# Optimization experiments

Measured on AMD Instinct MI355X. Metric: run time of the kernel, lower is better.

Reference implementation:

```python
import jax, jax.numpy as jnp
import numpy as np

B = 524288
IN_DIM = 16
OUT_DIM = 32  # hidden_dim3
N_CHUNKS = 4
CHUNK = 4


def ste_round(x):
    # straight-through round (grad passes unchanged, like Round.apply)
    return x + jax.lax.stop_gradient(jnp.round(x) - x)


def ste_sign(x):
    # straight-through sign (grad passes unchanged, like Sign.apply)
    return x + jax.lax.stop_gradient(jnp.sign(x) - x)


def setup_inputs() -> dict:
    key = jax.random.key(0)
    k1, k2 = jax.random.split(key)
    Input = jax.random.uniform(k1, (B, IN_DIM), dtype=jnp.float32)
    weight = jax.random.normal(k2, (OUT_DIM, IN_DIM), dtype=jnp.float32)
    InMin = jnp.float32(0.0)
    InMax = jnp.float32(1.0)
    return {"Input": Input, "weight": weight, "InMin": InMin, "InMax": InMax}


def reference(Input, weight, InMin, InMax):
    # eval-mode forward of QuantLinear
    scale = InMax - InMin
    w = ste_sign(weight)                       # [O, I] in {-1, 0, 1}
    wP = jax.nn.relu(w)                        # positive mask
    wM = jax.nn.relu(-w)                       # negative mask

    # 4-bit input quantization (eval path): clip(round((x-min)/(max-min)*15), 0, 15)
    q = jnp.clip(ste_round((Input - InMin) / scale * 15.0), 0.0, 15.0)  # [B, I]

    # bias = linear(InMin * ones, w): each row = InMin * sum_j w[o, j]
    bias = InMin * jnp.sum(w, axis=1)          # [O], broadcasts over batch

    # chunked 4-wide linears, vectorized over the 4 chunks
    qc = q.reshape(B, N_CHUNKS, CHUNK)         # [B, C, 4]
    wPc = wP.reshape(OUT_DIM, N_CHUNKS, CHUNK)  # [O, C, 4]
    wMc = wM.reshape(OUT_DIM, N_CHUNKS, CHUNK)
    yP = jnp.einsum('bcf,ocf->cbo', qc, wPc)   # [C, B, O]
    yM = jnp.einsum('bcf,ocf->cbo', qc, wMc)   # [C, B, O]

    # accumulate clip(round(y/15), -4, 4) * (InMax - InMin) over all 8 terms
    terms = jnp.clip(ste_round(yP / 15.0), -4.0, 4.0) \
          + jnp.clip(ste_round(-yM / 15.0), -4.0, 4.0)  # [C, B, O]
    x = jnp.sum(terms, axis=0) * scale + bias  # [B, O]
    return x
```

## Files before the change

### kernel.cpp

```cpp
#include <hip/hip_runtime.h>
#include <stdint.h>


#if __has_builtin(__builtin_amdgcn_udot4)
#define HAVE_UDOT4 1
#else
#define HAVE_UDOT4 0
#endif

typedef float f32x4 __attribute__((ext_vector_type(4)));

__device__ __forceinline__ int rnd15(int x) {
    return (int)(__umul24((unsigned)x, 274u) >> 12);
}

#if HAVE_UDOT4
#define TERM(q, mp, mm)                                                     \
    (rnd15((int)__builtin_amdgcn_udot4((q), (mp), 7u, false)) -             \
     rnd15((int)__builtin_amdgcn_udot4((q), (mm), 7u, false)))
#else
#define BSUM(x) ((int)((uint32_t)((x) * 0x01010101u) >> 24))
#define TERM(q, mp, mm)                                                     \
    (rnd15(BSUM((q) & (mp)) + 7) - rnd15(BSUM((q) & (mm)) + 7))
#endif

__global__ __launch_bounds__(256) void qlin_main(
    const float* __restrict__ in, const float* __restrict__ wgt,
    const float* __restrict__ pmin, const float* __restrict__ pmax,
    float* __restrict__ out, int nrows)
{
    __shared__ __align__(16) uint32_t cmP[128];
    __shared__ __align__(16) uint32_t cmM[128];
    __shared__ __align__(16) float sbias[32];
    __shared__ __align__(16) uint32_t xpose[256];

    const int t = threadIdx.x;
    const int lane = t & 63;
    const int wv = t >> 6;
    const size_t R0 = ((size_t)blockIdx.x * 4 + wv) * 64;
    (void)nrows;

    const float4* inp = (const float4*)in + R0 * 4 + lane;
    float4 f0 = inp[0], f1 = inp[64], f2 = inp[128], f3 = inp[192];

    const uint32_t MB = HAVE_UDOT4 ? 1u : 0xFFu;

    if (t < 128) {
        const int o = t >> 2, c = t & 3;
        const float* wrow = wgt + o * 16 + c * 4;
        uint32_t mp = 0, mm = 0;
#pragma unroll
        for (int j = 0; j < 4; ++j) {
            float v = wrow[j];
            if (v > 0.0f) mp |= MB << (8 * j);
            if (v < 0.0f) mm |= MB << (8 * j);
        }
        cmP[t] = mp;
        cmM[t] = mm;
    }
    if (t < 32) {
        const float* wrow = wgt + t * 16;
        int s = 0;
#pragma unroll
        for (int j = 0; j < 16; ++j) {
            float v = wrow[j];
            s += (v > 0.0f) ? 1 : 0;
            s -= (v < 0.0f) ? 1 : 0;
        }
        sbias[t] = __fmul_rn(pmin[0], (float)s);
    }
    __syncthreads();

    const int ogrp = lane & 7;
    const int rsel = lane >> 3;
    uint32_t* xp = xpose + (wv << 6);

    const uint4 P0 = *(const uint4*)&cmP[(ogrp * 4 + 0) * 4];
    const uint4 P1 = *(const uint4*)&cmP[(ogrp * 4 + 1) * 4];
    const uint4 P2 = *(const uint4*)&cmP[(ogrp * 4 + 2) * 4];
    const uint4 P3 = *(const uint4*)&cmP[(ogrp * 4 + 3) * 4];
    const uint4 M0 = *(const uint4*)&cmM[(ogrp * 4 + 0) * 4];
    const uint4 M1 = *(const uint4*)&cmM[(ogrp * 4 + 1) * 4];
    const uint4 M2 = *(const uint4*)&cmM[(ogrp * 4 + 2) * 4];
    const uint4 M3 = *(const uint4*)&cmM[(ogrp * 4 + 3) * 4];
    const float4 bias = *(const float4*)(sbias + ogrp * 4);

    const float InMin = pmin[0];
    const float scale = __fsub_rn(pmax[0], InMin);
    const bool unit =
        (__builtin_amdgcn_readfirstlane(__float_as_uint(scale)) == 0x3f800000u);

#define QUANT1(EJ, PK, J)                                                   \
        {                                                                   \
            float v  = __fmul_rn(EJ, 15.0f);                                \
            float rr = rintf(v);                                            \
            rr = fminf(fmaxf(rr, 0.0f), 15.0f);                             \
            PK |= ((uint32_t)(int)rr) << (8 * (J));                         \
        }

#define QUANT(F, QW)                                                        \
    {                                                                       \
        uint32_t pk = 0;                                                    \
        if (unit) {                                                         \
            QUANT1(__fsub_rn(F.x, InMin), pk, 0)                            \
            QUANT1(__fsub_rn(F.y, InMin), pk, 1)                            \
            QUANT1(__fsub_rn(F.z, InMin), pk, 2)                            \
            QUANT1(__fsub_rn(F.w, InMin), pk, 3)                            \
        } else {                                                            \
            QUANT1(__fdiv_rn(__fsub_rn(F.x, InMin), scale), pk, 0)          \
            QUANT1(__fdiv_rn(__fsub_rn(F.y, InMin), scale), pk, 1)          \
            QUANT1(__fdiv_rn(__fsub_rn(F.z, InMin), scale), pk, 2)          \
            QUANT1(__fdiv_rn(__fsub_rn(F.w, InMin), scale), pk, 3)          \
        }                                                                   \
        QW = pk;                                                            \
    }

#define ROWCOMP(q0, q1, q2, q3, dst)                                        \
        {                                                                   \
            int a0 = TERM(q0, P0.x, M0.x) + TERM(q1, P0.y, M0.y)            \
                   + TERM(q2, P0.z, M0.z) + TERM(q3, P0.w, M0.w);           \
            int a1 = TERM(q0, P1.x, M1.x) + TERM(q1, P1.y, M1.y)            \
                   + TERM(q2, P1.z, M1.z) + TERM(q3, P1.w, M1.w);           \
            int a2 = TERM(q0, P2.x, M2.x) + TERM(q1, P2.y, M2.y)            \
                   + TERM(q2, P2.z, M2.z) + TERM(q3, P2.w, M2.w);           \
            int a3 = TERM(q0, P3.x, M3.x) + TERM(q1, P3.y, M3.y)            \
                   + TERM(q2, P3.z, M3.z) + TERM(q3, P3.w, M3.w);           \
            f32x4 res;                                                      \
            res.x = __fadd_rn(__fmul_rn((float)a0, scale), bias.x);         \
            res.y = __fadd_rn(__fmul_rn((float)a1, scale), bias.y);         \
            res.z = __fadd_rn(__fmul_rn((float)a2, scale), bias.z);         \
            res.w = __fadd_rn(__fmul_rn((float)a3, scale), bias.w);         \
            __builtin_nontemporal_store(res, (f32x4*)(dst));                \
        }

#define SLAB(F, K)                                                          \
    {                                                                       \
        uint32_t qw;                                                        \
        QUANT(F, qw);                                                       \
        xp[lane] = qw;                                                      \
        const uint4 qA = *(const uint4*)(xp + (rsel << 2));                 \
        const uint4 qB = *(const uint4*)(xp + 32 + (rsel << 2));            \
        float* p0 = out + (R0 + (size_t)(K) * 16 + rsel) * 32 + (ogrp << 2);\
        ROWCOMP(qA.x, qA.y, qA.z, qA.w, p0);                                \
        ROWCOMP(qB.x, qB.y, qB.z, qB.w, p0 + 256);                          \
    }

    SLAB(f0, 0)
    SLAB(f1, 1)
    SLAB(f2, 2)
    SLAB(f3, 3)

#undef SLAB
#undef ROWCOMP
#undef QUANT
#undef QUANT1
}

extern "C" void kernel_launch(void* const* d_in, const int* in_sizes, int n_in,
                              void* d_out, int out_size, void* d_ws, size_t ws_size,
                              hipStream_t stream) {
    (void)n_in; (void)d_ws; (void)ws_size; (void)out_size;
    const float* in  = (const float*)d_in[0];
    const float* wgt = (const float*)d_in[1];
    const float* mn  = (const float*)d_in[2];
    const float* mx  = (const float*)d_in[3];
    float* out = (float*)d_out;
    const int nrows = in_sizes[0] / 16;
    const int blocks = nrows / 256;
    qlin_main<<<blocks, 256, 0, stream>>>(in, wgt, mn, mx, out, nrows);
}
```

Before: 100.5 us.

## Fold round-by-15 into udot4 weights and build per-wave masks without block barrier

Pre-scales the quantized inputs by 2 and uses 137 as each mask byte, so one udot4 with a folded bias constant plus a shift replaces the separate multiply-shift rounding step. Each wavefront now builds its own copy of the weight masks and the bias (computed with popcount) in shared memory, which removes the block-wide __syncthreads at the cost of redundant setup work and more LDS. Output stores also change from nontemporal to plain stores. The new exact-division trick relies on the udot4 sums staying small enough to avoid overflow and on the rounding identity holding across the full 0..60 range.

Result: no change. 98.63 us, median of 2 (-1.9%).

```diff
diff --git a/kernel.cpp b/kernel.cpp
--- a/kernel.cpp
+++ b/kernel.cpp
@@ -10,18 +10,23 @@
 
 typedef float f32x4 __attribute__((ext_vector_type(4)));
 
-__device__ __forceinline__ int rnd15(int x) {
+#if HAVE_UDOT4
+#define TERM(q2, mp, mm)                                                    \
+    ((int)(__builtin_amdgcn_udot4((q2), (mp), 1918u, false) >> 12) -        \
+     (int)(__builtin_amdgcn_udot4((q2), (mm), 1918u, false) >> 12))
+#define MBYTE 137u
+#define QSH 1
+#define BPB 3
+#else
+#define BSUM(x) ((int)((uint32_t)((x) * 0x01010101u) >> 24))
+__device__ __forceinline__ int rnd15f(int x) {
     return (int)(__umul24((unsigned)x, 274u) >> 12);
 }
-
-#if HAVE_UDOT4
 #define TERM(q, mp, mm)                                                     \
-    (rnd15((int)__builtin_amdgcn_udot4((q), (mp), 7u, false)) -             \
-     rnd15((int)__builtin_amdgcn_udot4((q), (mm), 7u, false)))
-#else
-#define BSUM(x) ((int)((uint32_t)((x) * 0x01010101u) >> 24))
-#define TERM(q, mp, mm)                                                     \
-    (rnd15(BSUM((q) & (mp)) + 7) - rnd15(BSUM((q) & (mm)) + 7))
+    (rnd15f(BSUM((q) & (mp)) + 7) - rnd15f(BSUM((q) & (mm)) + 7))
+#define MBYTE 0xFFu
+#define QSH 0
+#define BPB 8
 #endif
 
 __global__ __launch_bounds__(256) void qlin_main(
@@ -29,10 +34,10 @@
     const float* __restrict__ pmin, const float* __restrict__ pmax,
     float* __restrict__ out, int nrows)
 {
-    __shared__ __align__(16) uint32_t cmP[128];
-    __shared__ __align__(16) uint32_t cmM[128];
-    __shared__ __align__(16) float sbias[32];
-    __shared__ __align__(16) uint32_t xpose[256];
+    __shared__ __align__(16) uint32_t sP[4][128];
+    __shared__ __align__(16) uint32_t sM[4][128];
+    __shared__ __align__(16) float    sB[4][32];
+    __shared__ __align__(16) uint32_t sX[4][64];
 
     const int t = threadIdx.x;
     const int lane = t & 63;
@@ -43,47 +48,41 @@
     const float4* inp = (const float4*)in + R0 * 4 + lane;
     float4 f0 = inp[0], f1 = inp[64], f2 = inp[128], f3 = inp[192];
 
-    const uint32_t MB = HAVE_UDOT4 ? 1u : 0xFFu;
-
-    if (t < 128) {
-        const int o = t >> 2, c = t & 3;
-        const float* wrow = wgt + o * 16 + c * 4;
+#pragma unroll
+    for (int k = 0; k < 2; ++k) {
+        const int w = lane * 2 + k;
+        const float4 wf = *(const float4*)(wgt + w * 4);
         uint32_t mp = 0, mm = 0;
+        const float e[4] = { wf.x, wf.y, wf.z, wf.w };
 #pragma unroll
         for (int j = 0; j < 4; ++j) {
-            float v = wrow[j];
-            if (v > 0.0f) mp |= MB << (8 * j);
-            if (v < 0.0f) mm |= MB << (8 * j);
+            if (e[j] > 0.0f) mp |= MBYTE << (8 * j);
+            if (e[j] < 0.0f) mm |= MBYTE << (8 * j);
         }
-        cmP[t] = mp;
-        cmM[t] = mm;
+        sP[wv][w] = mp;
+        sM[wv][w] = mm;
     }
-    if (t < 32) {
-        const float* wrow = wgt + t * 16;
-        int s = 0;
+    if (lane < 32) {
+        int pc = 0;
 #pragma unroll
-        for (int j = 0; j < 16; ++j) {
-            float v = wrow[j];
-            s += (v > 0.0f) ? 1 : 0;
-            s -= (v < 0.0f) ? 1 : 0;
-        }
-        sbias[t] = __fmul_rn(pmin[0], (float)s);
+        for (int c = 0; c < 4; ++c)
+            pc += __popc(sP[wv][lane * 4 + c]) - __popc(sM[wv][lane * 4 + c]);
+        sB[wv][lane] = __fmul_rn(pmin[0], (float)(pc / BPB));
     }
-    __syncthreads();
 
     const int ogrp = lane & 7;
     const int rsel = lane >> 3;
-    uint32_t* xp = xpose + (wv << 6);
+    uint32_t* xp = sX[wv];
 
-    const uint4 P0 = *(const uint4*)&cmP[(ogrp * 4 + 0) * 4];
-    const uint4 P1 = *(const uint4*)&cmP[(ogrp * 4 + 1) * 4];
-    const uint4 P2 = *(const uint4*)&cmP[(ogrp * 4 + 2) * 4];
-    const uint4 P3 = *(const uint4*)&cmP[(ogrp * 4 + 3) * 4];
-    const uint4 M0 = *(const uint4*)&cmM[(ogrp * 4 + 0) * 4];
-    const uint4 M1 = *(const uint4*)&cmM[(ogrp * 4 + 1) * 4];
-    const uint4 M2 = *(const uint4*)&cmM[(ogrp * 4 + 2) * 4];
-    const uint4 M3 = *(const uint4*)&cmM[(ogrp * 4 + 3) * 4];
-    const float4 bias = *(const float4*)(sbias + ogrp * 4);
+    const uint4 P0 = *(const uint4*)&sP[wv][(ogrp * 4 + 0) * 4];
+    const uint4 P1 = *(const uint4*)&sP[wv][(ogrp * 4 + 1) * 4];
+    const uint4 P2 = *(const uint4*)&sP[wv][(ogrp * 4 + 2) * 4];
+    const uint4 P3 = *(const uint4*)&sP[wv][(ogrp * 4 + 3) * 4];
+    const uint4 M0 = *(const uint4*)&sM[wv][(ogrp * 4 + 0) * 4];
+    const uint4 M1 = *(const uint4*)&sM[wv][(ogrp * 4 + 1) * 4];
+    const uint4 M2 = *(const uint4*)&sM[wv][(ogrp * 4 + 2) * 4];
+    const uint4 M3 = *(const uint4*)&sM[wv][(ogrp * 4 + 3) * 4];
+    const float4 bias = *(const float4*)&sB[wv][ogrp * 4];
 
     const float InMin = pmin[0];
     const float scale = __fsub_rn(pmax[0], InMin);
@@ -95,7 +94,7 @@
             float v  = __fmul_rn(EJ, 15.0f);                                \
             float rr = rintf(v);                                            \
             rr = fminf(fmaxf(rr, 0.0f), 15.0f);                             \
-            PK |= ((uint32_t)(int)rr) << (8 * (J));                         \
+            PK |= ((uint32_t)(int)rr) << (8 * (J) + QSH);                   \
         }
 
 #define QUANT(F, QW)                                                        \
@@ -130,7 +129,7 @@
             res.y = __fadd_rn(__fmul_rn((float)a1, scale), bias.y);         \
             res.z = __fadd_rn(__fmul_rn((float)a2, scale), bias.z);         \
             res.w = __fadd_rn(__fmul_rn((float)a3, scale), bias.w);         \
-            __builtin_nontemporal_store(res, (f32x4*)(dst));                \
+            *(f32x4*)(dst) = res;                                           \
         }
 
 #define SLAB(F, K)                                                          \
```
